# Performance work log

Hardware: AMD Instinct MI355X
Metric: run time of the kernel (lower is better)

## Reference

```python
import jax, jax.numpy as jnp
import numpy as np

N = 100000
E = 1600000
EPS = 1e-5


def _layer_norm(x, g, b):
    mu = jnp.mean(x, axis=-1, keepdims=True)
    var = jnp.mean((x - mu) ** 2, axis=-1, keepdims=True)
    return (x - mu) * jax.lax.rsqrt(var + EPS) * g + b


def _sage(x, src, dst, wl, bl, wr):
    # mean aggregation of neighbor messages x[src] into dst, then linear
    msg_sum = jax.ops.segment_sum(x[src], dst, num_segments=N)          # [N, d_in]
    cnt = jax.ops.segment_sum(jnp.ones((src.shape[0],), x.dtype), dst, num_segments=N)
    mean = msg_sum / jnp.maximum(cnt, 1.0)[:, None]
    return mean @ wl.T + bl + x @ wr.T  # lin_l(mean) + lin_r(x), bias only on lin_l


def setup_inputs() -> dict:
    key = jax.random.key(0)
    ks = jax.random.split(key, 16)
    dims = [(9, 64), (64, 128), (128, 128), (128, 128)]
    inp = {
        "x": jax.random.normal(ks[0], (N, 9), dtype=jnp.float32),
        "edge_index": jax.random.randint(ks[1], (2, E), 0, N, dtype=jnp.int32),
    }
    for i, (din, dout) in enumerate(dims, start=1):
        s = 1.0 / np.sqrt(din)
        inp[f"w{i}l"] = jax.random.uniform(ks[2 + 3 * i], (dout, din), jnp.float32, -s, s)
        inp[f"b{i}"] = jnp.zeros((dout,), jnp.float32)
        inp[f"w{i}r"] = jax.random.uniform(ks[3 + 3 * i], (dout, din), jnp.float32, -s, s)
        inp[f"g{i}"] = jnp.ones((dout,), jnp.float32)
        inp[f"be{i}"] = jnp.zeros((dout,), jnp.float32)
    return inp


def reference(x, edge_index,
              w1l, b1, w1r, g1, be1,
              w2l, b2, w2r, g2, be2,
              w3l, b3, w3r, g3, be3,
              w4l, b4, w4r, g4, be4):
    src, dst = edge_index[0], edge_index[1]
    h = jax.nn.relu(_layer_norm(_sage(x, src, dst, w1l, b1, w1r), g1, be1))
    h = jax.nn.relu(_layer_norm(_sage(h, src, dst, w2l, b2, w2r), g2, be2))
    h = jax.nn.relu(_layer_norm(_sage(h, src, dst, w3l, b3, w3r), g3, be3))
    h = _layer_norm(_sage(h, src, dst, w4l, b4, w4r), g4, be4)
    return h
```

## Files before the change

kernel.cpp:

```cpp
#include <hip/hip_runtime.h>
#include <hip/hip_bf16.h>
#include <math.h>

#define N_NODES 100000
#define EPS 1e-5f
#define B2SH 11
#define NPB2 2048
#define NBUCK2 ((N_NODES + NPB2 - 1) / NPB2)
#define NPART 256

typedef __attribute__((ext_vector_type(8))) short bf16x8;
typedef __attribute__((ext_vector_type(4))) float f32x4;
typedef __attribute__((ext_vector_type(2))) float f32x2;
typedef __attribute__((ext_vector_type(4))) unsigned int u32x4;

__device__ __forceinline__ unsigned short fbits(float f) {
    __hip_bfloat16 h = __float2bfloat16(f);
    return *reinterpret_cast<unsigned short*>(&h);
}
__device__ __forceinline__ void stv(float* p, float y) { *p = y; }
__device__ __forceinline__ void stv(__hip_bfloat16* p, float y) { *p = __float2bfloat16(y); }
__device__ __forceinline__ unsigned char f8enc(float y) {
    return (unsigned char)((unsigned int)__builtin_amdgcn_cvt_pk_fp8_f32(y, y, 0, false) & 0xffu);
}

__global__ void part_hist(const int* __restrict__ dst, int E, int* __restrict__ blkhist) {
    __shared__ int h[NBUCK2];
    int b = blockIdx.x;
    int slice = (E + NPART - 1) / NPART;
    int s0 = b * slice;
    int s1 = min(E, s0 + slice);
    for (int i = threadIdx.x; i < NBUCK2; i += 256) h[i] = 0;
    __syncthreads();
    for (int e = s0 + threadIdx.x; e < s1; e += 256) atomicAdd(&h[dst[e] >> B2SH], 1);
    __syncthreads();
    for (int i = threadIdx.x; i < NBUCK2; i += 256) blkhist[i * NPART + b] = h[i];
}

__global__ void part_offsets(const int* __restrict__ blkhist, int* __restrict__ blkoffs,
                             int* __restrict__ bbase2, int* __restrict__ row_ptr, int E) {
    __shared__ int tot[NBUCK2];
    __shared__ int sbase[NBUCK2 + 1];
    int j = threadIdx.x;
    if (j < NBUCK2) {
        int run = 0;
#pragma unroll 8
        for (int b = 0; b < NPART; ++b) {
            blkoffs[j * NPART + b] = run;
            run += blkhist[j * NPART + b];
        }
        tot[j] = run;
    }
    __syncthreads();
    if (j == 0) {
        int run = 0;
        for (int i = 0; i < NBUCK2; ++i) {
            sbase[i] = run;
            run += tot[i];
        }
        sbase[NBUCK2] = run;
        row_ptr[N_NODES] = E;
    }
    __syncthreads();
    if (j <= NBUCK2) bbase2[j] = sbase[j];
    if (j < NBUCK2) {
        int base = sbase[j];
#pragma unroll 8
        for (int b = 0; b < NPART; ++b) blkoffs[j * NPART + b] += base;
    }
}

__global__ void part_scatter(const int* __restrict__ src, const int* __restrict__ dst, int E,
                             const int* __restrict__ blkoffs, unsigned int* __restrict__ pairs) {
    __shared__ int pos[NBUCK2];
    int b = blockIdx.x;
    int slice = (E + NPART - 1) / NPART;
    int s0 = b * slice;
    int s1 = min(E, s0 + slice);
    for (int i = threadIdx.x; i < NBUCK2; i += 256) pos[i] = blkoffs[i * NPART + b];
    __syncthreads();
    for (int e = s0 + threadIdx.x; e < s1; e += 256) {
        int d = dst[e];
        int jb = d >> B2SH;
        int p = atomicAdd(&pos[jb], 1);
        pairs[p] = ((unsigned int)src[e] << B2SH) | (unsigned int)(d & (NPB2 - 1));
    }
}

__global__ __launch_bounds__(1024) void bucket_build2(const unsigned int* __restrict__ pairs,
                                                      const int* __restrict__ bbase2,
                                                      int* __restrict__ row_ptr,
                                                      int* __restrict__ col) {
    __shared__ int lcnt[NPB2];
    __shared__ int lofs[NPB2];
    __shared__ int part[1024];
    int bk = blockIdx.x;
    int base = bbase2[bk];
    int cntb = bbase2[bk + 1] - base;
    int node0 = bk << B2SH;
    int t = threadIdx.x;
    lcnt[t] = 0;
    lcnt[t + 1024] = 0;
    __syncthreads();
    for (int i = t; i < cntb; i += 1024) atomicAdd(&lcnt[pairs[base + i] & (NPB2 - 1)], 1);
    __syncthreads();
    int a0 = lcnt[2 * t], a1 = lcnt[2 * t + 1];
    part[t] = a0 + a1;
    __syncthreads();
    for (int off = 1; off < 1024; off <<= 1) {
        int v = (t >= off) ? part[t - off] : 0;
        __syncthreads();
        part[t] += v;
        __syncthreads();
    }
    int excl = part[t] - (a0 + a1);
    lofs[2 * t] = excl;
    lofs[2 * t + 1] = excl + a0;
    __syncthreads();
#pragma unroll
    for (int k = 0; k < 2; ++k) {
        int ln = 2 * t + k;
        int node = node0 + ln;
        if (node < N_NODES) row_ptr[node] = base + lofs[ln];
    }
    lcnt[t] = 0;
    lcnt[t + 1024] = 0;
    __syncthreads();
    for (int i = t; i < cntb; i += 1024) {
        unsigned int v = pairs[base + i];
        int ld = v & (NPB2 - 1);
        int s = v >> B2SH;
        int p = base + lofs[ld] + atomicAdd(&lcnt[ld], 1);
        col[p] = s;
    }
}

__global__ void agg9_kernel(const float* __restrict__ x, const int* __restrict__ row_ptr,
                            const int* __restrict__ col, float* __restrict__ mean, int n) {
    int node = (blockIdx.x * blockDim.x + threadIdx.x) >> 6;
    int lane = threadIdx.x & 63;
    int wv = threadIdx.x >> 6;
    __shared__ float red[4][64];
    float acc = 0.f;
    int start = 0, end = 0;
    if (node < n) {
        start = row_ptr[node];
        end = row_ptr[node + 1];
        int g = lane / 9;
        int f = lane - g * 9;
        if (g < 7 && end > start) {
            for (int p = start + g; p < end; p += 28) {
#pragma unroll
                for (int i = 0; i < 4; ++i) {
                    int q = p + i * 7;
                    int idx = (q < end) ? q : end - 1;
                    float v = __builtin_nontemporal_load(&x[(size_t)col[idx] * 9 + f]);
                    if (q >= end) v = 0.f;
                    acc += v;
                }
            }
        }
    }
    red[wv][lane] = acc;
    __syncthreads();
    if (node < n && lane < 9) {
        float s = red[wv][lane];
#pragma unroll
        for (int k = 1; k < 7; ++k) s += red[wv][lane + 9 * k];
        float inv = 1.f / fmaxf((float)(end - start), 1.f);
        mean[(size_t)node * 9 + lane] = s * inv;
    }
}

__device__ __forceinline__ void acc16_fp8(const u32x4& v, float* acc) {
#pragma unroll
    for (int d = 0; d < 4; ++d) {
        unsigned int u = v[d];
        f32x2 a = __builtin_amdgcn_cvt_pk_f32_fp8(u, false);
        f32x2 b = __builtin_amdgcn_cvt_pk_f32_fp8(u, true);
        acc[d * 4 + 0] += a[0];
        acc[d * 4 + 1] += a[1];
        acc[d * 4 + 2] += b[0];
        acc[d * 4 + 3] += b[1];
    }
}

__global__ __launch_bounds__(256) void agg64_kernel(const unsigned char* __restrict__ h8,
                                                    const int* __restrict__ row_ptr,
                                                    const int* __restrict__ col,
                                                    unsigned short* __restrict__ mean, int n) {
    int node = (blockIdx.x * blockDim.x + threadIdx.x) >> 6;
    int lane = threadIdx.x & 63;
    if (node >= n) return;
    int e = lane >> 2, c = lane & 3;
    int start = row_ptr[node], end = row_ptr[node + 1];
    int deg = end - start;
    if (deg <= 0) {
        mean[(size_t)node * 64 + lane] = 0;
        return;
    }
    float acc[16];
#pragma unroll
    for (int j = 0; j < 16; ++j) acc[j] = 0.f;
    const unsigned char* hc = h8 + c * 16;
    for (int p = start; p < end; p += 32) {
        int qa = p + e;
        int qb = p + 16 + e;
        int ia = col[(qa < end) ? qa : end - 1];
        int ib = col[(qb < end) ? qb : end - 1];
        u32x4 va = __builtin_nontemporal_load((const u32x4*)(hc + ((size_t)ia << 6)));
        u32x4 vb = __builtin_nontemporal_load((const u32x4*)(hc + ((size_t)ib << 6)));
        if (qa >= end) va = (u32x4){0u, 0u, 0u, 0u};
        if (qb >= end) vb = (u32x4){0u, 0u, 0u, 0u};
        acc16_fp8(va, acc);
        acc16_fp8(vb, acc);
    }
#pragma unroll
    for (int j = 0; j < 16; ++j) {
        acc[j] += __shfl_xor(acc[j], 4);
        acc[j] += __shfl_xor(acc[j], 8);
        acc[j] += __shfl_xor(acc[j], 16);
        acc[j] += __shfl_xor(acc[j], 32);
    }
    if (e == 0) {
        float inv = 1.f / (float)deg;
        unsigned int w[8];
#pragma unroll
        for (int j = 0; j < 8; ++j) {
            unsigned int lo = fbits(acc[2 * j] * inv);
            unsigned int hi = fbits(acc[2 * j + 1] * inv);
            w[j] = lo | (hi << 16);
        }
        unsigned short* mrow = mean + (size_t)node * 64 + c * 16;
        *(uint4*)(mrow) = (uint4){w[0], w[1], w[2], w[3]};
        *(uint4*)(mrow + 8) = (uint4){w[4], w[5], w[6], w[7]};
    }
}

__global__ __launch_bounds__(256) void agg128_kernel(const unsigned char* __restrict__ h8,
                                                     const int* __restrict__ row_ptr,
                                                     const int* __restrict__ col,
                                                     unsigned short* __restrict__ mean, int n) {
    int node = (blockIdx.x * blockDim.x + threadIdx.x) >> 6;
    int lane = threadIdx.x & 63;
    if (node >= n) return;
    int e = lane >> 3, c = lane & 7;
    int start = row_ptr[node], end = row_ptr[node + 1];
    int deg = end - start;
    if (deg <= 0) {
        *(unsigned int*)&mean[(size_t)node * 128 + lane * 2] = 0u;
        return;
    }
    float acc[16];
#pragma unroll
    for (int j = 0; j < 16; ++j) acc[j] = 0.f;
    const unsigned char* hc = h8 + c * 16;
    for (int p = start; p < end; p += 32) {
        u32x4 v[4];
        bool m[4];
#pragma unroll
        for (int j = 0; j < 4; ++j) {
            int q = p + 8 * j + e;
            m[j] = q < end;
            int idx = col[m[j] ? q : end - 1];
            v[j] = __builtin_nontemporal_load((const u32x4*)(hc + ((size_t)idx << 7)));
        }
#pragma unroll
        for (int j = 0; j < 4; ++j) {
            if (!m[j]) v[j] = (u32x4){0u, 0u, 0u, 0u};
            acc16_fp8(v[j], acc);
        }
    }
#pragma unroll
    for (int j = 0; j < 16; ++j) {
        acc[j] += __shfl_xor(acc[j], 8);
        acc[j] += __shfl_xor(acc[j], 16);
        acc[j] += __shfl_xor(acc[j], 32);
    }
    if (e == 0) {
        float inv = 1.f / (float)deg;
        unsigned int w[8];
#pragma unroll
        for (int j = 0; j < 8; ++j) {
            unsigned int lo = fbits(acc[2 * j] * inv);
            unsigned int hi = fbits(acc[2 * j + 1] * inv);
            w[j] = lo | (hi << 16);
        }
        unsigned short* mrow = mean + (size_t)node * 128 + c * 16;
        *(uint4*)(mrow) = (uint4){w[0], w[1], w[2], w[3]};
        *(uint4*)(mrow + 8) = (uint4){w[4], w[5], w[6], w[7]};
    }
}

__global__ void wtrans_kernel(const float* __restrict__ wl, const float* __restrict__ wr,
                              int din, int dout, float* __restrict__ wt) {
    int i = blockIdx.x * blockDim.x + threadIdx.x;
    int K2 = 2 * din;
    if (i >= K2 * dout) return;
    int k = i / dout, j = i % dout;
    wt[k * dout + j] = (k < din) ? wl[j * din + k] : wr[j * din + (k - din)];
}

__global__ void packw_kernel(const float* __restrict__ wl, const float* __restrict__ wr,
                             int din, unsigned short* __restrict__ bpack) {
    int K2 = 2 * din;
    int total = K2 * 128;
    int i = blockIdx.x * 256 + threadIdx.x;
    if (i >= total) return;
    int e = i & 7;
    int lane = (i >> 3) & 63;
    int rest = i >> 9;
    int KSTEPS = din / 16;
    int t = rest / KSTEPS, ks = rest % KSTEPS;
    int j = t * 16 + (lane & 15);
    int k = ks * 32 + (lane >> 4) * 8 + e;
    float w = (k < din) ? wl[j * din + k] : wr[j * din + (k - din)];
    bpack[i] = fbits(w);
}

template <int DIN, int DOUT, bool RELU, typename OT>
__global__ __launch_bounds__(256) void linear_ln_kernel(
    const float* __restrict__ meanp, const float* __restrict__ hp,
    const float* __restrict__ wt, const float* __restrict__ bias,
    const float* __restrict__ g, const float* __restrict__ be,
    OT* __restrict__ out, unsigned char* __restrict__ out8, int n) {
    constexpr int K2 = 2 * DIN;
    constexpr int NCOL = DOUT / 4;
    constexpr int NROW = 256 / NCOL;
    constexpr int TN = 4 * NROW;
    constexpr int ASTR = TN + 4;
    constexpr int OSTR = DOUT + 4;
    constexpr int SMEMF = (K2 * ASTR > TN * OSTR) ? K2 * ASTR : TN * OSTR;
    __shared__ float smem[SMEMF];

    int tid = threadIdx.x;
    int n0base = blockIdx.x * TN;

    for (int idx = tid; idx < TN * K2; idx += 256) {
        int nn = idx / K2;
        int k = idx % K2;
        int node = n0base + nn;
        float v = 0.f;
        if (node < n)
            v = (k < DIN) ? meanp[(size_t)node * DIN + k] : hp[(size_t)node * DIN + (k - DIN)];
        smem[k * ASTR + nn] = v;
    }
    __syncthreads();

    int colt = tid % NCOL;
    int rowt = tid / NCOL;
    int j0 = colt * 4;
    int nn0 = rowt * 4;

    float acc[4][4];
#pragma unroll
    for (int i = 0; i < 4; ++i)
#pragma unroll
        for (int j = 0; j < 4; ++j) acc[i][j] = 0.f;

#pragma unroll 2
    for (int k = 0; k < K2; ++k) {
        float4 a = *(const float4*)&smem[k * ASTR + nn0];
        float4 w = *(const float4*)&wt[k * DOUT + j0];
        acc[0][0] = fmaf(a.x, w.x, acc[0][0]);
        acc[0][1] = fmaf(a.x, w.y, acc[0][1]);
        acc[0][2] = fmaf(a.x, w.z, acc[0][2]);
        acc[0][3] = fmaf(a.x, w.w, acc[0][3]);
        acc[1][0] = fmaf(a.y, w.x, acc[1][0]);
        acc[1][1] = fmaf(a.y, w.y, acc[1][1]);
        acc[1][2] = fmaf(a.y, w.z, acc[1][2]);
        acc[1][3] = fmaf(a.y, w.w, acc[1][3]);
        acc[2][0] = fmaf(a.z, w.x, acc[2][0]);
        acc[2][1] = fmaf(a.z, w.y, acc[2][1]);
        acc[2][2] = fmaf(a.z, w.z, acc[2][2]);
        acc[2][3] = fmaf(a.z, w.w, acc[2][3]);
        acc[3][0] = fmaf(a.w, w.x, acc[3][0]);
        acc[3][1] = fmaf(a.w, w.y, acc[3][1]);
        acc[3][2] = fmaf(a.w, w.z, acc[3][2]);
        acc[3][3] = fmaf(a.w, w.w, acc[3][3]);
    }
    __syncthreads();

    float4 bj = *(const float4*)&bias[j0];
#pragma unroll
    for (int i = 0; i < 4; ++i) {
        float4 o;
        o.x = acc[i][0] + bj.x;
        o.y = acc[i][1] + bj.y;
        o.z = acc[i][2] + bj.z;
        o.w = acc[i][3] + bj.w;
        *(float4*)&smem[(nn0 + i) * OSTR + j0] = o;
    }
    __syncthreads();

    int wid = tid >> 6, lane = tid & 63;
    for (int nn = wid; nn < TN; nn += 4) {
        int node = n0base + nn;
        if (node >= n) continue;
        float v0 = smem[nn * OSTR + lane];
        float v1 = (DOUT == 128) ? smem[nn * OSTR + 64 + lane] : 0.f;
        float s = v0 + v1;
        float ss = v0 * v0 + v1 * v1;
#pragma unroll
        for (int off = 32; off > 0; off >>= 1) {
            s += __shfl_xor(s, off);
            ss += __shfl_xor(ss, off);
        }
        float mu = s / DOUT;
        float var = ss / DOUT - mu * mu;
        float inv = rsqrtf(var + EPS);
        float y0 = (v0 - mu) * inv * g[lane] + be[lane];
        if (RELU) y0 = fmaxf(y0, 0.f);
        stv(&out[(size_t)node * DOUT + lane], y0);
        if (out8) out8[(size_t)node * DOUT + lane] = f8enc(y0);
        if (DOUT == 128) {
            float y1 = (v1 - mu) * inv * g[64 + lane] + be[64 + lane];
            if (RELU) y1 = fmaxf(y1, 0.f);
            stv(&out[(size_t)node * DOUT + 64 + lane], y1);
            if (out8) out8[(size_t)node * DOUT + 64 + lane] = f8enc(y1);
        }
    }
}

template <int DIN, bool RELU, typename OT>
__global__ __launch_bounds__(256) void mfma_linear_ln(
    const unsigned short* __restrict__ meanb, const unsigned short* __restrict__ hb,
    const unsigned short* __restrict__ bpack, const float* __restrict__ bias,
    const float* __restrict__ g, const float* __restrict__ be, OT* __restrict__ out,
    unsigned char* __restrict__ out8, int n) {
    constexpr int KSTEPS = DIN / 16;
    int tid = threadIdx.x;
    int w = tid >> 6, l = tid & 63;
    int n0 = blockIdx.x * 64 + w * 16;
    int arow = l & 15;
    int koff = (l >> 4) * 8;
    int anode = n0 + arow;
    if (anode >= n) anode = n - 1;
    const unsigned short* mrow = meanb + (size_t)anode * DIN;
    const unsigned short* hrow = hb + (size_t)anode * DIN;

    f32x4 acc[8];
#pragma unroll
    for (int t = 0; t < 8; ++t) acc[t] = (f32x4){0.f, 0.f, 0.f, 0.f};

#pragma unroll
    for (int ks = 0; ks < KSTEPS; ++ks) {
        int k = ks * 32 + koff;
        const unsigned short* ap = (k < DIN) ? (mrow + k) : (hrow + (k - DIN));
        bf16x8 a = *(const bf16x8*)ap;
#pragma unroll
        for (int t = 0; t < 8; ++t) {
            bf16x8 b = *(const bf16x8*)(bpack + (((size_t)t * KSTEPS + ks) * 64 + l) * 8);
            acc[t] = __builtin_amdgcn_mfma_f32_16x16x32_bf16(a, b, acc[t], 0, 0, 0);
        }
    }

    int jbase = l & 15;
    float bj[8], gj[8], bej[8];
#pragma unroll
    for (int t = 0; t < 8; ++t) {
        bj[t] = bias[t * 16 + jbase];
        gj[t] = g[t * 16 + jbase];
        bej[t] = be[t * 16 + jbase];
    }
#pragma unroll
    for (int r = 0; r < 4; ++r) {
        float v[8];
        float s = 0.f, ss = 0.f;
#pragma unroll
        for (int t = 0; t < 8; ++t) {
            v[t] = acc[t][r] + bj[t];
            s += v[t];
            ss += v[t] * v[t];
        }
#pragma unroll
        for (int off = 1; off < 16; off <<= 1) {
            s += __shfl_xor(s, off);
            ss += __shfl_xor(ss, off);
        }
        float mu = s * (1.f / 128.f);
        float var = ss * (1.f / 128.f) - mu * mu;
        float inv = rsqrtf(var + EPS);
        int node = n0 + (l >> 4) * 4 + r;
        if (node < n) {
#pragma unroll
            for (int t = 0; t < 8; ++t) {
                float y = (v[t] - mu) * inv * gj[t] + bej[t];
                if (RELU) y = fmaxf(y, 0.f);
                stv(&out[(size_t)node * 128 + t * 16 + jbase], y);
                if (out8) out8[(size_t)node * 128 + t * 16 + jbase] = f8enc(y);
            }
        }
    }
}

extern "C" void kernel_launch(void* const* d_in, const int* in_sizes, int n_in,
                              void* d_out, int out_size, void* d_ws, size_t ws_size,
                              hipStream_t stream) {
    const float* x = (const float*)d_in[0];
    const int* edge = (const int*)d_in[1];
    int E = in_sizes[1] / 2;
    const int* src = edge;
    const int* dst = edge + E;

    const float* w1l = (const float*)d_in[2];
    const float* b1  = (const float*)d_in[3];
    const float* w1r = (const float*)d_in[4];
    const float* g1  = (const float*)d_in[5];
    const float* be1 = (const float*)d_in[6];
    const float* w2l = (const float*)d_in[7];
    const float* b2  = (const float*)d_in[8];
    const float* w2r = (const float*)d_in[9];
    const float* g2  = (const float*)d_in[10];
    const float* be2 = (const float*)d_in[11];
    const float* w3l = (const float*)d_in[12];
    const float* b3  = (const float*)d_in[13];
    const float* w3r = (const float*)d_in[14];
    const float* g3  = (const float*)d_in[15];
    const float* be3 = (const float*)d_in[16];
    const float* w4l = (const float*)d_in[17];
    const float* b4  = (const float*)d_in[18];
    const float* w4r = (const float*)d_in[19];
    const float* g4  = (const float*)d_in[20];
    const float* be4 = (const float*)d_in[21];

    char* ws = (char*)d_ws;
    size_t off = 0;
    auto alloc = [&](size_t bytes) {
        void* p = ws + off;
        off = (off + bytes + 255) & ~(size_t)255;
        return p;
    };
    int* row_ptr = (int*)alloc((N_NODES + 1) * sizeof(int));
    int* blkhist = (int*)alloc((size_t)NBUCK2 * NPART * sizeof(int));
    int* blkoffs = (int*)alloc((size_t)NBUCK2 * NPART * sizeof(int));
    int* bbase2  = (int*)alloc((NBUCK2 + 1) * sizeof(int));
    unsigned int* pairs = (unsigned int*)alloc((size_t)E * sizeof(unsigned int));
    int* colx    = (int*)alloc(((size_t)E + 64) * sizeof(int));
    float* wt1   = (float*)alloc(18 * 64 * sizeof(float));
    unsigned short* bp2 = (unsigned short*)alloc(128 * 128 * sizeof(short));
    unsigned short* bp3 = (unsigned short*)alloc(256 * 128 * sizeof(short));
    unsigned short* bp4 = (unsigned short*)alloc(256 * 128 * sizeof(short));
    float* m9    = (float*)alloc((size_t)N_NODES * 9 * sizeof(float));
    unsigned short* mbf = (unsigned short*)alloc((size_t)N_NODES * 128 * sizeof(short));
    unsigned short* h1  = (unsigned short*)alloc((size_t)N_NODES * 64 * sizeof(short));
    unsigned short* h2  = (unsigned short*)alloc((size_t)N_NODES * 128 * sizeof(short));
    unsigned short* h3  = (unsigned short*)alloc((size_t)N_NODES * 128 * sizeof(short));
    unsigned char* h1f8 = (unsigned char*)alloc((size_t)N_NODES * 64);
    unsigned char* h2f8 = (unsigned char*)alloc((size_t)N_NODES * 128);
    unsigned char* h3f8 = (unsigned char*)alloc((size_t)N_NODES * 128);
    (void)ws_size;

    part_hist<<<NPART, 256, 0, stream>>>(dst, E, blkhist);
    part_offsets<<<1, 64, 0, stream>>>(blkhist, blkoffs, bbase2, row_ptr, E);
    part_scatter<<<NPART, 256, 0, stream>>>(src, dst, E, blkoffs, pairs);
    bucket_build2<<<NBUCK2, 1024, 0, stream>>>(pairs, bbase2, row_ptr, colx);

    wtrans_kernel<<<(18 * 64 + 255) / 256, 256, 0, stream>>>(w1l, w1r, 9, 64, wt1);
    packw_kernel<<<(128 * 128 + 255) / 256, 256, 0, stream>>>(w2l, w2r, 64, bp2);
    packw_kernel<<<(256 * 128 + 255) / 256, 256, 0, stream>>>(w3l, w3r, 128, bp3);
    packw_kernel<<<(256 * 128 + 255) / 256, 256, 0, stream>>>(w4l, w4r, 128, bp4);

    float* out = (float*)d_out;
    int AGB = (N_NODES * 64 + 255) / 256;
    int LNB = (N_NODES + 63) / 64;

    agg9_kernel<<<AGB, 256, 0, stream>>>(x, row_ptr, colx, m9, N_NODES);
    linear_ln_kernel<9, 64, true, __hip_bfloat16><<<LNB, 256, 0, stream>>>(
        m9, x, wt1, b1, g1, be1, (__hip_bfloat16*)h1, h1f8, N_NODES);
    agg64_kernel<<<AGB, 256, 0, stream>>>(h1f8, row_ptr, colx, mbf, N_NODES);
    mfma_linear_ln<64, true, __hip_bfloat16><<<LNB, 256, 0, stream>>>(
        mbf, h1, bp2, b2, g2, be2, (__hip_bfloat16*)h2, h2f8, N_NODES);
    agg128_kernel<<<AGB, 256, 0, stream>>>(h2f8, row_ptr, colx, mbf, N_NODES);
    mfma_linear_ln<128, true, __hip_bfloat16><<<LNB, 256, 0, stream>>>(
        mbf, h2, bp3, b3, g3, be3, (__hip_bfloat16*)h3, h3f8, N_NODES);
    agg128_kernel<<<AGB, 256, 0, stream>>>(h3f8, row_ptr, colx, mbf, N_NODES);
    mfma_linear_ln<128, false, float><<<LNB, 256, 0, stream>>>(
        mbf, h3, bp4, b4, g4, be4, out, (unsigned char*)nullptr, N_NODES);
}
```

Baseline: 424.7 us.

## Shrink CSR buckets, rewrite agg64 per-lane byte gather, drop nontemporal loads

The CSR build now uses 512-node buckets with 256-thread blocks instead of 2048-node buckets with 1024 threads, which gives more, smaller blocks. The agg64 kernel gathers with one lane per feature byte and a single accumulator, replacing the 16-byte vector loads per lane and the shuffle reduction. Nontemporal loads are removed in agg9 and agg128 so gathered rows can stay in cache. Byte-wise gathers in agg64 issue many more load instructions per edge, and part_offsets now launches 256 threads, which assumes that kernel copes with the larger bucket count.

```diff
diff --git a/kernel.cpp b/kernel.cpp
--- a/kernel.cpp
+++ b/kernel.cpp
@@ -4,8 +4,8 @@
 
 #define N_NODES 100000
 #define EPS 1e-5f
-#define B2SH 11
-#define NPB2 2048
+#define B2SH 9
+#define NPB2 512
 #define NBUCK2 ((N_NODES + NPB2 - 1) / NPB2)
 #define NPART 256
 
@@ -87,27 +87,27 @@
     }
 }
 
-__global__ __launch_bounds__(1024) void bucket_build2(const unsigned int* __restrict__ pairs,
-                                                      const int* __restrict__ bbase2,
-                                                      int* __restrict__ row_ptr,
-                                                      int* __restrict__ col) {
+__global__ __launch_bounds__(256) void bucket_build2(const unsigned int* __restrict__ pairs,
+                                                     const int* __restrict__ bbase2,
+                                                     int* __restrict__ row_ptr,
+                                                     int* __restrict__ col) {
     __shared__ int lcnt[NPB2];
     __shared__ int lofs[NPB2];
-    __shared__ int part[1024];
+    __shared__ int part[256];
     int bk = blockIdx.x;
     int base = bbase2[bk];
     int cntb = bbase2[bk + 1] - base;
     int node0 = bk << B2SH;
     int t = threadIdx.x;
     lcnt[t] = 0;
-    lcnt[t + 1024] = 0;
-    __syncthreads();
-    for (int i = t; i < cntb; i += 1024) atomicAdd(&lcnt[pairs[base + i] & (NPB2 - 1)], 1);
+    lcnt[t + 256] = 0;
+    __syncthreads();
+    for (int i = t; i < cntb; i += 256) atomicAdd(&lcnt[pairs[base + i] & (NPB2 - 1)], 1);
     __syncthreads();
     int a0 = lcnt[2 * t], a1 = lcnt[2 * t + 1];
     part[t] = a0 + a1;
     __syncthreads();
-    for (int off = 1; off < 1024; off <<= 1) {
+    for (int off = 1; off < 256; off <<= 1) {
         int v = (t >= off) ? part[t - off] : 0;
         __syncthreads();
         part[t] += v;
@@ -124,9 +124,9 @@
         if (node < N_NODES) row_ptr[node] = base + lofs[ln];
     }
     lcnt[t] = 0;
-    lcnt[t + 1024] = 0;
-    __syncthreads();
-    for (int i = t; i < cntb; i += 1024) {
+    lcnt[t + 256] = 0;
+    __syncthreads();
+    for (int i = t; i < cntb; i += 256) {
         unsigned int v = pairs[base + i];
         int ld = v & (NPB2 - 1);
         int s = v >> B2SH;
@@ -154,7 +154,7 @@
                 for (int i = 0; i < 4; ++i) {
                     int q = p + i * 7;
                     int idx = (q < end) ? q : end - 1;
-                    float v = __builtin_nontemporal_load(&x[(size_t)col[idx] * 9 + f]);
+                    float v = x[(size_t)col[idx] * 9 + f];
                     if (q >= end) v = 0.f;
                     acc += v;
                 }
@@ -192,49 +192,34 @@
     int node = (blockIdx.x * blockDim.x + threadIdx.x) >> 6;
     int lane = threadIdx.x & 63;
     if (node >= n) return;
-    int e = lane >> 2, c = lane & 3;
     int start = row_ptr[node], end = row_ptr[node + 1];
     int deg = end - start;
     if (deg <= 0) {
         mean[(size_t)node * 64 + lane] = 0;
         return;
     }
-    float acc[16];
-#pragma unroll
-    for (int j = 0; j < 16; ++j) acc[j] = 0.f;
-    const unsigned char* hc = h8 + c * 16;
-    for (int p = start; p < end; p += 32) {
-        int qa = p + e;
-        int qb = p + 16 + e;
-        int ia = col[(qa < end) ? qa : end - 1];
-        int ib = col[(qb < end) ? qb : end - 1];
-        u32x4 va = __builtin_nontemporal_load((const u32x4*)(hc + ((size_t)ia << 6)));
-        u32x4 vb = __builtin_nontemporal_load((const u32x4*)(hc + ((size_t)ib << 6)));
-        if (qa >= end) va = (u32x4){0u, 0u, 0u, 0u};
-        if (qb >= end) vb = (u32x4){0u, 0u, 0u, 0u};
-        acc16_fp8(va, acc);
-        acc16_fp8(vb, acc);
-    }
-#pragma unroll
-    for (int j = 0; j < 16; ++j) {
-        acc[j] += __shfl_xor(acc[j], 4);
-        acc[j] += __shfl_xor(acc[j], 8);
-        acc[j] += __shfl_xor(acc[j], 16);
-        acc[j] += __shfl_xor(acc[j], 32);
-    }
-    if (e == 0) {
-        float inv = 1.f / (float)deg;
-        unsigned int w[8];
-#pragma unroll
-        for (int j = 0; j < 8; ++j) {
-            unsigned int lo = fbits(acc[2 * j] * inv);
-            unsigned int hi = fbits(acc[2 * j + 1] * inv);
-            w[j] = lo | (hi << 16);
-        }
-        unsigned short* mrow = mean + (size_t)node * 64 + c * 16;
-        *(uint4*)(mrow) = (uint4){w[0], w[1], w[2], w[3]};
-        *(uint4*)(mrow + 8) = (uint4){w[4], w[5], w[6], w[7]};
-    }
+    const unsigned char* hl = h8 + lane;
+    float acc = 0.f;
+    int p = start;
+    int nfull = start + (deg & ~7);
+    for (; p < nfull; p += 8) {
+#pragma unroll
+        for (int i = 0; i < 8; ++i) {
+            unsigned int off = (unsigned int)col[p + i] << 6;
+            acc += __builtin_amdgcn_cvt_f32_fp8((unsigned int)hl[off], 0);
+        }
+    }
+    if (p < end) {
+#pragma unroll
+        for (int i = 0; i < 8; ++i) {
+            int q = p + i;
+            int idx = (q < end) ? q : p;
+            unsigned int off = (unsigned int)col[idx] << 6;
+            float v = __builtin_amdgcn_cvt_f32_fp8((unsigned int)hl[off], 0);
+            if (q < end) acc += v;
+        }
+    }
+    mean[(size_t)node * 64 + lane] = fbits(acc / (float)deg);
 }
 
 __global__ __launch_bounds__(256) void agg128_kernel(const unsigned char* __restrict__ h8,
@@ -263,7 +248,7 @@
             int q = p + 8 * j + e;
             m[j] = q < end;
             int idx = col[m[j] ? q : end - 1];
-            v[j] = __builtin_nontemporal_load((const u32x4*)(hc + ((size_t)idx << 7)));
+            v[j] = *(const u32x4*)(hc + ((size_t)idx << 7));
         }
 #pragma unroll
         for (int j = 0; j < 4; ++j) {
@@ -552,9 +537,9 @@
     (void)ws_size;
 
     part_hist<<<NPART, 256, 0, stream>>>(dst, E, blkhist);
-    part_offsets<<<1, 64, 0, stream>>>(blkhist, blkoffs, bbase2, row_ptr, E);
+    part_offsets<<<1, 256, 0, stream>>>(blkhist, blkoffs, bbase2, row_ptr, E);
     part_scatter<<<NPART, 256, 0, stream>>>(src, dst, E, blkoffs, pairs);
-    bucket_build2<<<NBUCK2, 1024, 0, stream>>>(pairs, bbase2, row_ptr, colx);
+    bucket_build2<<<NBUCK2, 256, 0, stream>>>(pairs, bbase2, row_ptr, colx);
 
     wtrans_kernel<<<(18 * 64 + 255) / 256, 256, 0, stream>>>(w1l, w1r, 9, 64, wt1);
     packw_kernel<<<(128 * 128 + 255) / 256, 256, 0, stream>>>(w2l, w2r, 64, bp2);
```

New measurement: 391.3 us. -7.9%, faster.
